# Kernel tuning notes

Measured on AMD Instinct MI355X. Metric: run time of the kernel, lower is better.

## Reference

```python
import jax, jax.numpy as jnp
import numpy as np

EPS = 1e-7

def _cell(x_t, h, s_l, s_B, lambda_log, B):
    # x_t: [b, d], h/s_l: [b, n], s_B: [b, n, d], lambda_log: [n], B: [n, d]
    lam = jnp.exp(-jnp.exp(lambda_log))                    # [n]
    gamma = jnp.sqrt(1.0 - lam * lam + EPS)                # [n]
    Bx = x_t @ B.T                                         # [b, n]
    h1 = lam * h + gamma * Bx
    dlam = -lam * jnp.exp(lambda_log)                      # d lambda / d lambda_log
    s_l1 = h * dlam + lam * s_l + Bx * (-lam / gamma) * dlam
    s_B1 = lam[None, :, None] * s_B + gamma[None, :, None] * x_t[:, None, :]
    return h1, s_l1, s_B1

def setup_inputs() -> dict:
    key = jax.random.key(0)
    k1, k2, k3, k4 = jax.random.split(key, 4)
    S, BT, D, N, O = 256, 32, 128, 128, 128
    x = jax.random.normal(k1, (S, BT, D), dtype=jnp.float32)
    # torch init: lambda_log = log(-0.5*log(u1)) with rmin=0, rmax=1
    u1 = jax.random.uniform(k2, (N,), dtype=jnp.float32, minval=0.01, maxval=0.99)
    lambda_log = jnp.log(-0.5 * jnp.log(u1))
    B = jax.random.normal(k3, (N, D), dtype=jnp.float32) / np.sqrt(D)
    C = jax.random.normal(k4, (O, N), dtype=jnp.float32) / np.sqrt(N)
    return {"x": x, "lambda_log": lambda_log, "B": B, "C": C}

def reference(x, lambda_log, B, C):
    S, BT, D = x.shape
    N = B.shape[0]
    h0 = jnp.zeros((BT, N), x.dtype)
    sl0 = jnp.zeros((BT, N), x.dtype)
    sB0 = jnp.zeros((BT, N, D), x.dtype)

    def scan_fn(carry, x_t):
        h, s_l, s_B = carry
        h1, s_l1, s_B1 = _cell(x_t, h, s_l, s_B, lambda_log, B)
        return (h1, s_l1, s_B1), h1

    (hT, _, _), hs = jax.lax.scan(scan_fn, (h0, sl0, sB0), x)
    outputs = jnp.einsum('sbn,on->sbo', hs, C)  # h_t @ C^T per step
    return outputs, hT
```

## Files before the change

kernel.cpp:

```cpp
#include <hip/hip_runtime.h>

#define S_DIM 256
#define BT_DIM 32
#define D_DIM 128
#define N_DIM 128
#define O_DIM 128
#define SB (S_DIM * BT_DIM)
#define EPS 1e-7f

typedef short s16x8 __attribute__((ext_vector_type(8)));
typedef float fx4   __attribute__((ext_vector_type(4)));

union U8 { unsigned short u[8]; s16x8 v; };

__device__ __forceinline__ unsigned short f2bf(float f) {
    unsigned u = __builtin_bit_cast(unsigned, f);
    return (unsigned short)((u + 0x7fffu + ((u >> 16) & 1u)) >> 16);
}
__device__ __forceinline__ float bf2f(unsigned short h) {
    unsigned u = ((unsigned)h) << 16;
    return __builtin_bit_cast(float, u);
}
__device__ __forceinline__ s16x8 cvt8hi(const float4 f0, const float4 f1) {
    float f[8] = {f0.x, f0.y, f0.z, f0.w, f1.x, f1.y, f1.z, f1.w};
    U8 h;
    #pragma unroll
    for (int i = 0; i < 8; ++i) h.u[i] = f2bf(f[i]);
    return h.v;
}
__device__ __forceinline__ void pack4(const float4 f, unsigned* hi2, unsigned* lo2) {
    float f_[4] = {f.x, f.y, f.z, f.w};
    unsigned short hb[4], lb[4];
    #pragma unroll
    for (int i = 0; i < 4; ++i) {
        hb[i] = f2bf(f_[i]);
        lb[i] = f2bf(f_[i] - bf2f(hb[i]));
    }
    hi2[0] = (unsigned)hb[0] | ((unsigned)hb[1] << 16);
    hi2[1] = (unsigned)hb[2] | ((unsigned)hb[3] << 16);
    lo2[0] = (unsigned)lb[0] | ((unsigned)lb[1] << 16);
    lo2[1] = (unsigned)lb[2] | ((unsigned)lb[3] << 16);
}

__global__ __launch_bounds__(256) void k1_gemm_scan(const float* __restrict__ X,
                                                    const float* __restrict__ lamlog,
                                                    const float* __restrict__ Bm,
                                                    const float* __restrict__ Cm,
                                                    unsigned short* __restrict__ hs_hi,
                                                    unsigned short* __restrict__ Chi,
                                                    unsigned short* __restrict__ Clo,
                                                    float* __restrict__ hT) {
    const int t = threadIdx.x;

    if (blockIdx.x >= 256) {
        const int id = (blockIdx.x - 256) * 256 + t;
        const float4 f0 = reinterpret_cast<const float4*>(Cm)[id * 2];
        const float4 f1 = reinterpret_cast<const float4*>(Cm)[id * 2 + 1];
        unsigned h0[2], l0[2], h1[2], l1[2];
        pack4(f0, h0, l0);
        pack4(f1, h1, l1);
        *reinterpret_cast<uint4*>(Chi + (size_t)id * 8) = make_uint4(h0[0], h0[1], h1[0], h1[1]);
        *reinterpret_cast<uint4*>(Clo + (size_t)id * 8) = make_uint4(l0[0], l0[1], l1[0], l1[1]);
        return;
    }

    __shared__ unsigned short Bhi[16][136];
    __shared__ unsigned short Blo[16][136];
    __shared__ float Bxs[S_DIM][17];
    __shared__ float carr[16][17];

    const int b  = blockIdx.x >> 3;
    const int n0 = (blockIdx.x & 7) * 16;

    #pragma unroll
    for (int q = 0; q < 2; ++q) {
        const int id4 = t + 256 * q;
        const int row = id4 >> 5, c4 = id4 & 31;
        const float4 f = *reinterpret_cast<const float4*>(Bm + (size_t)(n0 + row) * D_DIM + c4 * 4);
        unsigned hi2[2], lo2[2];
        pack4(f, hi2, lo2);
        *reinterpret_cast<uint2*>(&Bhi[row][c4 * 4]) = make_uint2(hi2[0], hi2[1]);
        *reinterpret_cast<uint2*>(&Blo[row][c4 * 4]) = make_uint2(lo2[0], lo2[1]);
    }
    __syncthreads();

    const int w  = t >> 6, l = t & 63;
    const int lr = l & 15;
    const int lk = (l >> 4) * 8;

    s16x8 bh[4], bl[4];
    #pragma unroll
    for (int sl = 0; sl < 4; ++sl) {
        bh[sl] = *reinterpret_cast<const s16x8*>(&Bhi[lr][sl * 32 + lk]);
        bl[sl] = *reinterpret_cast<const s16x8*>(&Blo[lr][sl * 32 + lk]);
    }

    const float* __restrict__ xb = X + (size_t)b * D_DIM;
    #pragma unroll
    for (int q = 0; q < 4; ++q) {
        const int s0 = (w * 4 + q) * 16;
        const float* __restrict__ xr = xb + (size_t)(s0 + lr) * (BT_DIM * D_DIM);
        s16x8 ah[4];
        #pragma unroll
        for (int sl = 0; sl < 4; ++sl) {
            const float4 f0 = *reinterpret_cast<const float4*>(xr + sl * 32 + lk);
            const float4 f1 = *reinterpret_cast<const float4*>(xr + sl * 32 + lk + 4);
            ah[sl] = cvt8hi(f0, f1);
        }
        fx4 acc = {0.f, 0.f, 0.f, 0.f};
        #pragma unroll
        for (int sl = 0; sl < 4; ++sl) {
            acc = __builtin_amdgcn_mfma_f32_16x16x32_bf16(ah[sl], bh[sl], acc, 0, 0, 0);
            acc = __builtin_amdgcn_mfma_f32_16x16x32_bf16(ah[sl], bl[sl], acc, 0, 0, 0);
        }
        #pragma unroll
        for (int r = 0; r < 4; ++r)
            Bxs[s0 + (l >> 4) * 4 + r][lr] = acc[r];
    }
    __syncthreads();

    const int j = t & 15;
    const int c = t >> 4;
    const float ll    = lamlog[n0 + j];
    const float lam   = expf(-expf(ll));
    const float gamma = sqrtf(1.f - lam * lam + EPS);
    const float l2 = lam * lam, l4 = l2 * l2, l8 = l4 * l4;
    const float lam16 = l8 * l8;

    float h = 0.f;
    #pragma unroll
    for (int i = 0; i < 16; ++i)
        h = fmaf(lam, h, gamma * Bxs[c * 16 + i][j]);
    carr[c][j] = h;
    __syncthreads();

    float Hb = 0.f;
    for (int cp = 0; cp < c; ++cp)
        Hb = fmaf(lam16, Hb, carr[cp][j]);

    h = Hb;
    #pragma unroll
    for (int i = 0; i < 16; ++i) {
        h = fmaf(lam, h, gamma * Bxs[c * 16 + i][j]);
        const size_t rg = (size_t)(c * 16 + i) * BT_DIM + b;
        hs_hi[rg * N_DIM + n0 + j] = f2bf(h);
    }
    if (c == 15) hT[b * N_DIM + n0 + j] = h;
}

__global__ __launch_bounds__(256) void k2_outgemm(const unsigned short* __restrict__ hs_hi,
                                                  const unsigned short* __restrict__ Chi,
                                                  const unsigned short* __restrict__ Clo,
                                                  float* __restrict__ out) {
    const int t  = threadIdx.x;
    const int r0 = blockIdx.x * 32;
    const int w  = t >> 6, l = t & 63;
    const int lr = l & 15;
    const int lk = (l >> 4) * 8;
    const int rbase = r0 + 16 * (w & 1) + lr;

    s16x8 ah[4];
    #pragma unroll
    for (int sl = 0; sl < 4; ++sl)
        ah[sl] = *reinterpret_cast<const s16x8*>(&hs_hi[(size_t)rbase * N_DIM + sl * 32 + lk]);

    #pragma unroll
    for (int q = 0; q < 4; ++q) {
        const int o0 = (w >> 1) * 64 + q * 16;
        fx4 acc = {0.f, 0.f, 0.f, 0.f};
        #pragma unroll
        for (int sl = 0; sl < 4; ++sl) {
            const s16x8 bh = *reinterpret_cast<const s16x8*>(&Chi[(size_t)(o0 + lr) * N_DIM + sl * 32 + lk]);
            const s16x8 bl = *reinterpret_cast<const s16x8*>(&Clo[(size_t)(o0 + lr) * N_DIM + sl * 32 + lk]);
            acc = __builtin_amdgcn_mfma_f32_16x16x32_bf16(ah[sl], bh, acc, 0, 0, 0);
            acc = __builtin_amdgcn_mfma_f32_16x16x32_bf16(ah[sl], bl, acc, 0, 0, 0);
        }
        const int rw = r0 + 16 * (w & 1) + (l >> 4) * 4;
        #pragma unroll
        for (int r = 0; r < 4; ++r)
            out[(size_t)(rw + r) * O_DIM + o0 + lr] = acc[r];
    }
}

extern "C" void kernel_launch(void* const* d_in, const int* in_sizes, int n_in,
                              void* d_out, int out_size, void* d_ws, size_t ws_size,
                              hipStream_t stream) {
    const float* x          = (const float*)d_in[0];
    const float* lambda_log = (const float*)d_in[1];
    const float* B          = (const float*)d_in[2];
    const float* C          = (const float*)d_in[3];

    float* out = (float*)d_out;
    float* hT  = out + (size_t)SB * O_DIM;

    unsigned short* hs_hi = (unsigned short*)d_ws;
    unsigned short* Chi   = hs_hi + (size_t)SB * N_DIM;
    unsigned short* Clo   = Chi + O_DIM * N_DIM;

    k1_gemm_scan<<<264, 256, 0, stream>>>(x, lambda_log, B, C, hs_hi, Chi, Clo, hT);
    k2_outgemm<<<256, 256, 0, stream>>>(hs_hi, Chi, Clo, out);
}
```

Measured before the change: 73.91 us.

## Fuse scan and output GEMM into one kernel via last-block atomic counter

Merges the two kernels into one. Each of the 8 blocks per batch element bumps an atomic counter when its scan finishes, and the last block to arrive computes that batch's output GEMM. The C hi/lo split is now done in registers inside that block instead of being precomputed to workspace. This removes one kernel launch and the gap between kernels, but adds a memset, and only 32 blocks (one per batch) do the whole output GEMM, so that phase runs with much less parallelism.

```diff
diff --git a/kernel.cpp b/kernel.cpp
--- a/kernel.cpp
+++ b/kernel.cpp
@@ -28,6 +28,17 @@
     for (int i = 0; i < 8; ++i) h.u[i] = f2bf(f[i]);
     return h.v;
 }
+__device__ __forceinline__ void cvt8(const float4 f0, const float4 f1, s16x8& hi, s16x8& lo) {
+    float f[8] = {f0.x, f0.y, f0.z, f0.w, f1.x, f1.y, f1.z, f1.w};
+    U8 h, l;
+    #pragma unroll
+    for (int i = 0; i < 8; ++i) {
+        unsigned short hb = f2bf(f[i]);
+        h.u[i] = hb;
+        l.u[i] = f2bf(f[i] - bf2f(hb));
+    }
+    hi = h.v; lo = l.v;
+}
 __device__ __forceinline__ void pack4(const float4 f, unsigned* hi2, unsigned* lo2) {
     float f_[4] = {f.x, f.y, f.z, f.w};
     unsigned short hb[4], lb[4];
@@ -42,33 +53,21 @@
     lo2[1] = (unsigned)lb[2] | ((unsigned)lb[3] << 16);
 }
 
-__global__ __launch_bounds__(256) void k1_gemm_scan(const float* __restrict__ X,
-                                                    const float* __restrict__ lamlog,
-                                                    const float* __restrict__ Bm,
-                                                    const float* __restrict__ Cm,
-                                                    unsigned short* __restrict__ hs_hi,
-                                                    unsigned short* __restrict__ Chi,
-                                                    unsigned short* __restrict__ Clo,
-                                                    float* __restrict__ hT) {
-    const int t = threadIdx.x;
-
-    if (blockIdx.x >= 256) {
-        const int id = (blockIdx.x - 256) * 256 + t;
-        const float4 f0 = reinterpret_cast<const float4*>(Cm)[id * 2];
-        const float4 f1 = reinterpret_cast<const float4*>(Cm)[id * 2 + 1];
-        unsigned h0[2], l0[2], h1[2], l1[2];
-        pack4(f0, h0, l0);
-        pack4(f1, h1, l1);
-        *reinterpret_cast<uint4*>(Chi + (size_t)id * 8) = make_uint4(h0[0], h0[1], h1[0], h1[1]);
-        *reinterpret_cast<uint4*>(Clo + (size_t)id * 8) = make_uint4(l0[0], l0[1], l1[0], l1[1]);
-        return;
-    }
-
+__global__ __launch_bounds__(256) void fused_lru(const float* __restrict__ X,
+                                                 const float* __restrict__ lamlog,
+                                                 const float* __restrict__ Bm,
+                                                 const float* __restrict__ Cm,
+                                                 unsigned* __restrict__ cnt,
+                                                 unsigned short* __restrict__ hs_hi,
+                                                 float* __restrict__ out,
+                                                 float* __restrict__ hT) {
     __shared__ unsigned short Bhi[16][136];
     __shared__ unsigned short Blo[16][136];
     __shared__ float Bxs[S_DIM][17];
     __shared__ float carr[16][17];
-
+    __shared__ int is_last;
+
+    const int t  = threadIdx.x;
     const int b  = blockIdx.x >> 3;
     const int n0 = (blockIdx.x & 7) * 16;
 
@@ -88,97 +87,112 @@
     const int lr = l & 15;
     const int lk = (l >> 4) * 8;
 
-    s16x8 bh[4], bl[4];
-    #pragma unroll
-    for (int sl = 0; sl < 4; ++sl) {
-        bh[sl] = *reinterpret_cast<const s16x8*>(&Bhi[lr][sl * 32 + lk]);
-        bl[sl] = *reinterpret_cast<const s16x8*>(&Blo[lr][sl * 32 + lk]);
-    }
-
-    const float* __restrict__ xb = X + (size_t)b * D_DIM;
-    #pragma unroll
-    for (int q = 0; q < 4; ++q) {
-        const int s0 = (w * 4 + q) * 16;
-        const float* __restrict__ xr = xb + (size_t)(s0 + lr) * (BT_DIM * D_DIM);
+    {
+        s16x8 bh[4], bl[4];
+        #pragma unroll
+        for (int sl = 0; sl < 4; ++sl) {
+            bh[sl] = *reinterpret_cast<const s16x8*>(&Bhi[lr][sl * 32 + lk]);
+            bl[sl] = *reinterpret_cast<const s16x8*>(&Blo[lr][sl * 32 + lk]);
+        }
+
+        const float* __restrict__ xb = X + (size_t)b * D_DIM;
+        #pragma unroll
+        for (int q = 0; q < 4; ++q) {
+            const int s0 = (w * 4 + q) * 16;
+            const float* __restrict__ xr = xb + (size_t)(s0 + lr) * (BT_DIM * D_DIM);
+            s16x8 ah[4];
+            #pragma unroll
+            for (int sl = 0; sl < 4; ++sl) {
+                const float4 f0 = *reinterpret_cast<const float4*>(xr + sl * 32 + lk);
+                const float4 f1 = *reinterpret_cast<const float4*>(xr + sl * 32 + lk + 4);
+                ah[sl] = cvt8hi(f0, f1);
+            }
+            fx4 acc = {0.f, 0.f, 0.f, 0.f};
+            #pragma unroll
+            for (int sl = 0; sl < 4; ++sl) {
+                acc = __builtin_amdgcn_mfma_f32_16x16x32_bf16(ah[sl], bh[sl], acc, 0, 0, 0);
+                acc = __builtin_amdgcn_mfma_f32_16x16x32_bf16(ah[sl], bl[sl], acc, 0, 0, 0);
+            }
+            #pragma unroll
+            for (int r = 0; r < 4; ++r)
+                Bxs[s0 + (l >> 4) * 4 + r][lr] = acc[r];
+        }
+    }
+    __syncthreads();
+
+    {
+        const int j = t & 15;
+        const int c = t >> 4;
+        const float ll    = lamlog[n0 + j];
+        const float lam   = expf(-expf(ll));
+        const float gamma = sqrtf(1.f - lam * lam + EPS);
+        const float l2 = lam * lam, l4 = l2 * l2, l8 = l4 * l4;
+        const float lam16 = l8 * l8;
+
+        float h = 0.f;
+        #pragma unroll
+        for (int i = 0; i < 16; ++i)
+            h = fmaf(lam, h, gamma * Bxs[c * 16 + i][j]);
+        carr[c][j] = h;
+        __syncthreads();
+
+        float Hb = 0.f;
+        for (int cp = 0; cp < c; ++cp)
+            Hb = fmaf(lam16, Hb, carr[cp][j]);
+
+        h = Hb;
+        #pragma unroll
+        for (int i = 0; i < 16; ++i) {
+            h = fmaf(lam, h, gamma * Bxs[c * 16 + i][j]);
+            const size_t rg = (size_t)(c * 16 + i) * BT_DIM + b;
+            hs_hi[rg * N_DIM + n0 + j] = f2bf(h);
+        }
+        if (c == 15) hT[b * N_DIM + n0 + j] = h;
+    }
+
+    __syncthreads();
+    __threadfence();
+    __syncthreads();
+    if (t == 0) is_last = (atomicAdd(&cnt[b], 1u) == 7u) ? 1 : 0;
+    __syncthreads();
+    if (!is_last) return;
+    __threadfence();
+
+    s16x8 ch[2][4], cl[2][4];
+    #pragma unroll
+    for (int j2 = 0; j2 < 2; ++j2) {
+        const int o0 = (2 * w + j2) * 16;
+        const float* __restrict__ cr = Cm + (size_t)(o0 + lr) * N_DIM;
+        #pragma unroll
+        for (int sl = 0; sl < 4; ++sl) {
+            const float4 f0 = *reinterpret_cast<const float4*>(cr + sl * 32 + lk);
+            const float4 f1 = *reinterpret_cast<const float4*>(cr + sl * 32 + lk + 4);
+            cvt8(f0, f1, ch[j2][sl], cl[j2][sl]);
+        }
+    }
+
+    for (int q16 = 0; q16 < 16; ++q16) {
+        const unsigned short* __restrict__ hr =
+            hs_hi + ((size_t)(q16 * 16 + lr) * BT_DIM + b) * N_DIM;
         s16x8 ah[4];
         #pragma unroll
-        for (int sl = 0; sl < 4; ++sl) {
-            const float4 f0 = *reinterpret_cast<const float4*>(xr + sl * 32 + lk);
-            const float4 f1 = *reinterpret_cast<const float4*>(xr + sl * 32 + lk + 4);
-            ah[sl] = cvt8hi(f0, f1);
-        }
-        fx4 acc = {0.f, 0.f, 0.f, 0.f};
-        #pragma unroll
-        for (int sl = 0; sl < 4; ++sl) {
-            acc = __builtin_amdgcn_mfma_f32_16x16x32_bf16(ah[sl], bh[sl], acc, 0, 0, 0);
-            acc = __builtin_amdgcn_mfma_f32_16x16x32_bf16(ah[sl], bl[sl], acc, 0, 0, 0);
-        }
-        #pragma unroll
-        for (int r = 0; r < 4; ++r)
-            Bxs[s0 + (l >> 4) * 4 + r][lr] = acc[r];
-    }
-    __syncthreads();
-
-    const int j = t & 15;
-    const int c = t >> 4;
-    const float ll    = lamlog[n0 + j];
-    const float lam   = expf(-expf(ll));
-    const float gamma = sqrtf(1.f - lam * lam + EPS);
-    const float l2 = lam * lam, l4 = l2 * l2, l8 = l4 * l4;
-    const float lam16 = l8 * l8;
-
-    float h = 0.f;
-    #pragma unroll
-    for (int i = 0; i < 16; ++i)
-        h = fmaf(lam, h, gamma * Bxs[c * 16 + i][j]);
-    carr[c][j] = h;
-    __syncthreads();
-
-    float Hb = 0.f;
-    for (int cp = 0; cp < c; ++cp)
-        Hb = fmaf(lam16, Hb, carr[cp][j]);
-
-    h = Hb;
-    #pragma unroll
-    for (int i = 0; i < 16; ++i) {
-        h = fmaf(lam, h, gamma * Bxs[c * 16 + i][j]);
-        const size_t rg = (size_t)(c * 16 + i) * BT_DIM + b;
-        hs_hi[rg * N_DIM + n0 + j] = f2bf(h);
-    }
-    if (c == 15) hT[b * N_DIM + n0 + j] = h;
-}
-
-__global__ __launch_bounds__(256) void k2_outgemm(const unsigned short* __restrict__ hs_hi,
-                                                  const unsigned short* __restrict__ Chi,
-                                                  const unsigned short* __restrict__ Clo,
-                                                  float* __restrict__ out) {
-    const int t  = threadIdx.x;
-    const int r0 = blockIdx.x * 32;
-    const int w  = t >> 6, l = t & 63;
-    const int lr = l & 15;
-    const int lk = (l >> 4) * 8;
-    const int rbase = r0 + 16 * (w & 1) + lr;
-
-    s16x8 ah[4];
-    #pragma unroll
-    for (int sl = 0; sl < 4; ++sl)
-        ah[sl] = *reinterpret_cast<const s16x8*>(&hs_hi[(size_t)rbase * N_DIM + sl * 32 + lk]);
-
-    #pragma unroll
-    for (int q = 0; q < 4; ++q) {
-        const int o0 = (w >> 1) * 64 + q * 16;
-        fx4 acc = {0.f, 0.f, 0.f, 0.f};
-        #pragma unroll
-        for (int sl = 0; sl < 4; ++sl) {
-            const s16x8 bh = *reinterpret_cast<const s16x8*>(&Chi[(size_t)(o0 + lr) * N_DIM + sl * 32 + lk]);
-            const s16x8 bl = *reinterpret_cast<const s16x8*>(&Clo[(size_t)(o0 + lr) * N_DIM + sl * 32 + lk]);
-            acc = __builtin_amdgcn_mfma_f32_16x16x32_bf16(ah[sl], bh, acc, 0, 0, 0);
-            acc = __builtin_amdgcn_mfma_f32_16x16x32_bf16(ah[sl], bl, acc, 0, 0, 0);
-        }
-        const int rw = r0 + 16 * (w & 1) + (l >> 4) * 4;
-        #pragma unroll
-        for (int r = 0; r < 4; ++r)
-            out[(size_t)(rw + r) * O_DIM + o0 + lr] = acc[r];
+        for (int sl = 0; sl < 4; ++sl)
+            ah[sl] = *reinterpret_cast<const s16x8*>(&hr[sl * 32 + lk]);
+
+        #pragma unroll
+        for (int j2 = 0; j2 < 2; ++j2) {
+            fx4 acc = {0.f, 0.f, 0.f, 0.f};
+            #pragma unroll
+            for (int sl = 0; sl < 4; ++sl) {
+                acc = __builtin_amdgcn_mfma_f32_16x16x32_bf16(ah[sl], ch[j2][sl], acc, 0, 0, 0);
+                acc = __builtin_amdgcn_mfma_f32_16x16x32_bf16(ah[sl], cl[j2][sl], acc, 0, 0, 0);
+            }
+            const int o0 = (2 * w + j2) * 16;
+            const int sw = q16 * 16 + (l >> 4) * 4;
+            #pragma unroll
+            for (int r = 0; r < 4; ++r)
+                out[((size_t)(sw + r) * BT_DIM + b) * O_DIM + o0 + lr] = acc[r];
+        }
     }
 }
 
@@ -193,10 +207,9 @@
     float* out = (float*)d_out;
     float* hT  = out + (size_t)SB * O_DIM;
 
-    unsigned short* hs_hi = (unsigned short*)d_ws;
-    unsigned short* Chi   = hs_hi + (size_t)SB * N_DIM;
-    unsigned short* Clo   = Chi + O_DIM * N_DIM;
-
-    k1_gemm_scan<<<264, 256, 0, stream>>>(x, lambda_log, B, C, hs_hi, Chi, Clo, hT);
-    k2_outgemm<<<256, 256, 0, stream>>>(hs_hi, Chi, Clo, out);
-}
+    unsigned* cnt = (unsigned*)d_ws;
+    unsigned short* hs_hi = (unsigned short*)((char*)d_ws + 256);
+
+    hipMemsetAsync(cnt, 0, 128, stream);
+    fused_lru<<<256, 256, 0, stream>>>(x, lambda_log, B, C, cnt, hs_hi, out, hT);
+}
```

Measured after the change: 112.9 us. +52.8%, slower.
